# Performance work log

Measured on AMD Instinct MI355X. Metric: run time of the kernel, lower is better.

## Reference

```python
import jax, jax.numpy as jnp
import numpy as np

B, S, SQ, N, DIN, H, A, O = 32, 1024, 32, 128, 128, 256, 100, 2000
MEM_COUNT, ANS_COUNT = 3, 2


def _gru_cell(x, h, w_ih, w_hh, b_ih, b_hh):
    # PyTorch GRUCell math
    gi = x @ w_ih.T + b_ih
    gh = h @ w_hh.T + b_hh
    i_r, i_z, i_n = jnp.split(gi, 3, axis=-1)
    h_r, h_z, h_n = jnp.split(gh, 3, axis=-1)
    r = jax.nn.sigmoid(i_r + h_r)
    z = jax.nn.sigmoid(i_z + h_z)
    n = jnp.tanh(i_n + r * h_n)
    return (1.0 - z) * n + z * h


def _gru_seq(x, h0, w_ih, w_hh, b_ih, b_hh):
    def step(h, xt):
        hn = _gru_cell(xt, h, w_ih, w_hh, b_ih, b_hh)
        return hn, hn
    hT, ys = jax.lax.scan(step, h0, jnp.swapaxes(x, 0, 1))
    return jnp.swapaxes(ys, 0, 1), hT


def setup_inputs() -> dict:
    key = jax.random.key(0)
    ks = iter(jax.random.split(key, 40))
    def U(shape, a=0.05):
        return jax.random.uniform(next(ks), shape, minval=-a, maxval=a, dtype=jnp.float32)
    inp = {}
    inp['c'] = jax.random.normal(next(ks), (B, S, DIN), dtype=jnp.float32)
    inp['q'] = jax.random.normal(next(ks), (B, SQ, DIN), dtype=jnp.float32)
    inp['i_state'] = jnp.zeros((1, B, H), jnp.float32)
    inp['q_state'] = jnp.zeros((1, B, H), jnp.float32)
    for p in ['in', 'qe']:
        inp[p + '_w_ih'] = U((3 * H, DIN)); inp[p + '_w_hh'] = U((3 * H, H))
        inp[p + '_b_ih'] = U((3 * H,)); inp[p + '_b_hh'] = U((3 * H,))
    inp['att_weight'] = U((H, H))
    inp['att_w1'] = U((A, 7 * H + 2)); inp['att_b1'] = U((A,))
    inp['att_w2'] = U((1, A)); inp['att_b2'] = U((1,))
    inp['mem_w_ih'] = U((3 * H, H)); inp['mem_w_hh'] = U((3 * H, H))
    inp['mem_b_ih'] = U((3 * H,)); inp['mem_b_hh'] = U((3 * H,))
    inp['out_w'] = U((O, H)); inp['out_b'] = U((O,))
    inp['ans_w_ih'] = U((3 * H, O + H)); inp['ans_w_hh'] = U((3 * H, H))
    inp['ans_b_ih'] = U((3 * H,)); inp['ans_b_hh'] = U((3 * H,))
    inp['c_index'] = jnp.sort(jax.random.randint(next(ks), (B, N), 0, S), axis=1)
    inp['len_c'] = jax.random.randint(next(ks), (B,), 1, N + 1)
    return inp


def reference(c, q, i_state, q_state, in_w_ih, in_w_hh, in_b_ih, in_b_hh,
              qe_w_ih, qe_w_hh, qe_b_ih, qe_b_hh, att_weight,
              att_w1, att_b1, att_w2, att_b2,
              mem_w_ih, mem_w_hh, mem_b_ih, mem_b_hh,
              out_w, out_b, ans_w_ih, ans_w_hh, ans_b_ih, ans_b_hh,
              c_index, len_c):
    # input / question GRU encoders (dropout omitted: eval mode)
    c_out, _ = _gru_seq(c, i_state[0], in_w_ih, in_w_hh, in_b_ih, in_b_hh)
    _, q_hT = _gru_seq(q, q_state[0], qe_w_ih, qe_w_hh, qe_b_ih, qe_b_hh)
    q_h = q_hT[:, None, :]                                   # [B,1,H]
    # gather sentence-end hidden states: [B,N,H]
    c_sel = jnp.take_along_axis(c_out, c_index[:, :, None], axis=1)
    n_sent = c_index.shape[1]
    mask = jnp.arange(n_sent)[None, :] < len_c[:, None]      # [B,N]
    cw = c_sel @ att_weight                                   # [B,N,H] (fixed across hops)
    m = q_h
    att_list = []
    for _ in range(MEM_COUNT):
        dot_q = (cw * q_h).sum(-1)                            # [B,N]
        dot_m = (cw * m).sum(-1)                              # [B,N]
        feats = jnp.concatenate([
            c_sel, jnp.broadcast_to(m, c_sel.shape), jnp.broadcast_to(q_h, c_sel.shape),
            c_sel * q_h, c_sel * m, jnp.abs(c_sel - q_h), jnp.abs(c_sel - m),
            dot_q[..., None], dot_m[..., None]], axis=2)      # [B,N,7H+2]
        h1 = jnp.tanh(feats @ att_w1.T + att_b1)
        scores = (h1 @ att_w2.T + att_b2)[..., 0]             # [B,N]
        p = jax.nn.softmax(jnp.where(mask, scores, -jnp.inf), axis=1)
        p = jnp.where(mask, p, 0.0)                           # zero-pad like pad_sequence
        att_list.append(p[..., None])
        e = (c_sel * p[..., None]).sum(1)                     # [B,H]
        m = _gru_cell(e, m[:, 0, :], mem_w_ih, mem_w_hh, mem_b_ih, mem_b_hh)[:, None, :]
    msq = m[:, 0, :]
    for _ in range(ANS_COUNT):
        y = jax.nn.softmax(msq @ out_w.T + out_b, axis=1)
        msq = _gru_cell(jnp.concatenate([y, q_hT], axis=1), msq,
                        ans_w_ih, ans_w_hh, ans_b_ih, ans_b_hh)
    y = jax.nn.softmax(msq @ out_w.T + out_b, axis=1)
    return y, jnp.stack(att_list)
```

## Files before the change

### kernel.cpp

```cpp
#include <hip/hip_runtime.h>
#include <cstdint>
#include <cstddef>

typedef short bf16x8 __attribute__((ext_vector_type(8)));
typedef float f32x4 __attribute__((ext_vector_type(4)));
typedef int   i32x4 __attribute__((ext_vector_type(4)));

#define DEV static __device__ __forceinline__

DEV unsigned short f2bf(float x){
  union{float f; unsigned int u;} v; v.f = x;
  unsigned int r = (v.u + 0x7FFFu + ((v.u>>16)&1u)) >> 16;
  return (unsigned short)r;
}
DEV float bf2f(unsigned short h){
  union{unsigned int u; float f;} v; v.u = ((unsigned int)h)<<16;
  return v.f;
}
DEV float bfsel(int dw, int hi){
  union{unsigned int u; float f;} v;
  v.u = hi ? ((unsigned int)dw & 0xFFFF0000u) : ((unsigned int)dw << 16);
  return v.f;
}
DEV float sigm_f(float x){ return __builtin_amdgcn_rcpf(1.0f + __expf(-x)); }
DEV float tanh_f(float x){ return 2.0f*__builtin_amdgcn_rcpf(1.0f + __expf(-2.0f*x)) - 1.0f; }

__global__ void k_f2bf(const float* __restrict__ src, unsigned short* __restrict__ dst, int n){
  int i = blockIdx.x*256 + threadIdx.x;
  if(i<n) dst[i] = f2bf(src[i]);
}

__global__ void k_transpose(const float* __restrict__ in, float* __restrict__ out, int R, int C){
  int i = blockIdx.x*256 + threadIdx.x;
  if(i < R*C){ int r = i/C, c = i - r*C; out[(size_t)c*R + r] = in[i]; }
}

__global__ void k_attw1(const float* __restrict__ w1, unsigned short* __restrict__ dst){
  int i = blockIdx.x*256 + threadIdx.x;
  if(i < 128*1824){
    int r = i/1824, cc = i - r*1824;
    float v = (r<100 && cc<1794)? w1[r*1794 + cc] : 0.0f;
    dst[i] = f2bf(v);
  }
}

__global__ void k_attwT(const float* __restrict__ aw, unsigned short* __restrict__ dst){
  int i = blockIdx.x*256 + threadIdx.x;
  if(i<65536){ int n = i>>8, k = i&255; dst[i] = f2bf(aw[k*256 + n]); }
}

__global__ void k_b1pad(const float* __restrict__ b1, float* __restrict__ dst){
  int i = threadIdx.x; if(i<128) dst[i] = (i<100)? b1[i] : 0.0f;
}

__global__ void k_copy(const float* __restrict__ s, float* __restrict__ d, int n){
  int i = blockIdx.x*256+threadIdx.x; if(i<n) d[i]=s[i];
}

__global__ __launch_bounds__(256) void k_gemm_bf16(
    const unsigned short* __restrict__ A, const unsigned short* __restrict__ Bt,
    int K, const float* __restrict__ bias, int act,
    float* __restrict__ outf, unsigned short* __restrict__ outbf, int ldc)
{
  int lane = threadIdx.x & 63, wave = threadIdx.x >> 6;
  int m_base = blockIdx.x*64 + (wave>>1)*32;
  int n_base = blockIdx.y*64 + (wave&1)*32;
  int cl = lane & 15, q4 = lane >> 4;
  f32x4 acc00={0.f,0.f,0.f,0.f}, acc01=acc00, acc10=acc00, acc11=acc00;
  const int kf_n = K >> 5;
  for(int kf=0; kf<kf_n; kf++){
    int ko = kf*32 + q4*8;
    bf16x8 a0 = *(const bf16x8*)(A + (size_t)(m_base+cl)*K + ko);
    bf16x8 a1 = *(const bf16x8*)(A + (size_t)(m_base+16+cl)*K + ko);
    bf16x8 b0 = *(const bf16x8*)(Bt + (size_t)(n_base+cl)*K + ko);
    bf16x8 b1 = *(const bf16x8*)(Bt + (size_t)(n_base+16+cl)*K + ko);
    acc00 = __builtin_amdgcn_mfma_f32_16x16x32_bf16(a0,b0,acc00,0,0,0);
    acc01 = __builtin_amdgcn_mfma_f32_16x16x32_bf16(a0,b1,acc01,0,0,0);
    acc10 = __builtin_amdgcn_mfma_f32_16x16x32_bf16(a1,b0,acc10,0,0,0);
    acc11 = __builtin_amdgcn_mfma_f32_16x16x32_bf16(a1,b1,acc11,0,0,0);
  }
  #pragma unroll
  for(int mt=0; mt<2; mt++){
    #pragma unroll
    for(int nt=0; nt<2; nt++){
      f32x4 av = (mt==0)? (nt==0?acc00:acc01) : (nt==0?acc10:acc11);
      int col = n_base + nt*16 + cl;
      float bv = bias? bias[col] : 0.0f;
      #pragma unroll
      for(int r=0;r<4;r++){
        int row = m_base + mt*16 + q4*4 + r;
        float v = av[r] + bv;
        if(act) v = tanh_f(v);
        if(outbf) outbf[(size_t)row*ldc + col] = f2bf(v);
        else      outf [(size_t)row*ldc + col] = v;
      }
    }
  }
}

__global__ __launch_bounds__(256) void k_gemm_gi(
    const unsigned short* __restrict__ A, const unsigned short* __restrict__ Bt,
    const float* __restrict__ bias, unsigned short* __restrict__ gi_out, int ss)
{
  int lane = threadIdx.x & 63, wave = threadIdx.x >> 6;
  int m_base = blockIdx.x*64 + (wave>>1)*32;
  int n_base = blockIdx.y*64 + (wave&1)*32;
  int cl = lane & 15, q4 = lane >> 4;
  f32x4 acc00={0.f,0.f,0.f,0.f}, acc01=acc00, acc10=acc00, acc11=acc00;
  for(int kf=0; kf<4; kf++){
    int ko = kf*32 + q4*8;
    bf16x8 a0 = *(const bf16x8*)(A + (size_t)(m_base+cl)*128 + ko);
    bf16x8 a1 = *(const bf16x8*)(A + (size_t)(m_base+16+cl)*128 + ko);
    bf16x8 b0 = *(const bf16x8*)(Bt + (size_t)(n_base+cl)*128 + ko);
    bf16x8 b1 = *(const bf16x8*)(Bt + (size_t)(n_base+16+cl)*128 + ko);
    acc00 = __builtin_amdgcn_mfma_f32_16x16x32_bf16(a0,b0,acc00,0,0,0);
    acc01 = __builtin_amdgcn_mfma_f32_16x16x32_bf16(a0,b1,acc01,0,0,0);
    acc10 = __builtin_amdgcn_mfma_f32_16x16x32_bf16(a1,b0,acc10,0,0,0);
    acc11 = __builtin_amdgcn_mfma_f32_16x16x32_bf16(a1,b1,acc11,0,0,0);
  }
  const int tmask = (1<<ss) - 1;
  #pragma unroll
  for(int mt=0; mt<2; mt++){
    #pragma unroll
    for(int nt=0; nt<2; nt++){
      f32x4 av = (mt==0)? (nt==0?acc00:acc01) : (nt==0?acc10:acc11);
      int col = n_base + nt*16 + cl;
      float bv = bias[col];
      int g = col >> 8, rem = col & 255;
      int w = rem >> 5, s = (rem>>4)&1, cl2 = rem & 15;
      #pragma unroll
      for(int r=0;r<4;r++){
        int arow = m_base + mt*16 + q4*4 + r;
        int t = arow & tmask, b = arow >> ss;
        int blk = b >> 4, brow = b & 15;
        int lane2 = (brow>>2)*16 + cl2, rc = brow & 3;
        size_t idx = ((((size_t)t*2 + blk)*8 + w)*64 + lane2)*24 + g*8 + s*4 + rc;
        gi_out[idx] = f2bf(av[r] + bv);
      }
    }
  }
}

__global__ __launch_bounds__(512,1) void k_gru_rec(
    const unsigned short* __restrict__ whh_c, const unsigned short* __restrict__ whh_q,
    const unsigned short* __restrict__ gi_c,  const unsigned short* __restrict__ gi_q,
    const float* __restrict__ bhh_c, const float* __restrict__ bhh_q,
    const float* __restrict__ h0_c,  const float* __restrict__ h0_q,
    float* __restrict__ c_out, float* __restrict__ q_hT)
{
  __shared__ unsigned short hb0[16*264];
  __shared__ unsigned short hb1[16*264];

  const int blk = blockIdx.x;
  const bool isq = blk >= 2;
  const int cls = isq? blk-2 : blk;
  const int b0 = cls * 16;
  const unsigned short* W  = isq? whh_q : whh_c;
  const unsigned short* GI = isq? gi_q  : gi_c;
  const float* bhh = isq? bhh_q : bhh_c;
  const float* h0  = isq? h0_q  : h0_c;
  const int steps  = isq? 32 : 1024;

  const int tid = threadIdx.x;
  const int lane = tid & 63, wave = tid >> 6;
  const int cl = lane & 15, q4 = lane >> 4;

  bf16x8 Bf[3][2][8];
  #pragma unroll
  for(int g=0; g<3; g++)
    #pragma unroll
    for(int s=0; s<2; s++){
      const unsigned short* wrow = W + (size_t)(g*256 + wave*32 + s*16 + cl)*256;
      #pragma unroll
      for(int kf=0; kf<8; kf++)
        Bf[g][s][kf] = *(const bf16x8*)(wrow + kf*32 + q4*8);
    }

  float bR[2], bZ[2], bN[2];
  #pragma unroll
  for(int s=0; s<2; s++){
    const int col = wave*32 + s*16 + cl;
    bR[s] = bhh[col]; bZ[s] = bhh[256+col]; bN[s] = bhh[512+col];
  }

  float hreg[2][4];
  #pragma unroll
  for(int s=0; s<2; s++){
    const int col = wave*32 + s*16 + cl;
    #pragma unroll
    for(int r=0; r<4; r++){
      const int row = q4*4 + r;
      float v = h0[(size_t)(b0+row)*256 + col];
      hreg[s][r] = v;
      hb0[row*264 + col] = f2bf(v);
    }
  }
  __syncthreads();

  unsigned short* hb_rd = hb0;
  unsigned short* hb_wr = hb1;

  const unsigned short* gi_lane = GI + (((size_t)cls*8 + wave)*64 + lane)*24;
  const size_t gi_tstride = (size_t)2*8*64*24;

  for(int t=0; t<steps; t++){
    const unsigned short* gp = gi_lane + (size_t)t*gi_tstride;
    i32x4 G0 = *(const i32x4*)(gp);
    i32x4 G1 = *(const i32x4*)(gp + 8);
    i32x4 G2 = *(const i32x4*)(gp + 16);

    if(!isq && t>0){
      #pragma unroll
      for(int s=0; s<2; s++){
        const int col = wave*32 + s*16 + cl;
        #pragma unroll
        for(int r=0; r<4; r++)
          c_out[((size_t)(b0+q4*4+r)*1024 + (t-1))*256 + col] = hreg[s][r];
      }
    }

    f32x4 acc[3][2];
    #pragma unroll
    for(int g=0; g<3; g++)
      #pragma unroll
      for(int s=0; s<2; s++){ f32x4 z={0.f,0.f,0.f,0.f}; acc[g][s]=z; }
    #pragma unroll
    for(int kf=0; kf<8; kf++){
      bf16x8 a = *(const bf16x8*)&hb_rd[cl*264 + kf*32 + q4*8];
      #pragma unroll
      for(int g=0; g<3; g++)
        #pragma unroll
        for(int s=0; s<2; s++)
          acc[g][s] = __builtin_amdgcn_mfma_f32_16x16x32_bf16(a, Bf[g][s][kf], acc[g][s], 0,0,0);
    }

    #pragma unroll
    for(int s=0; s<2; s++){
      const int col = wave*32 + s*16 + cl;
      #pragma unroll
      for(int r=0; r<4; r++){
        const int row = q4*4 + r;
        const int k = s*4 + r;
        float gir = bfsel(G0[k>>1], k&1);
        float giz = bfsel(G1[k>>1], k&1);
        float gin = bfsel(G2[k>>1], k&1);
        float rr = sigm_f(gir + acc[0][s][r] + bR[s]);
        float zz = sigm_f(giz + acc[1][s][r] + bZ[s]);
        float nn = tanh_f(gin + rr*(acc[2][s][r] + bN[s]));
        float x  = nn + zz*(hreg[s][r] - nn);
        hreg[s][r] = x;
        hb_wr[row*264 + col] = f2bf(x);
      }
    }
    __syncthreads();
    unsigned short* tmp = hb_rd; hb_rd = hb_wr; hb_wr = tmp;
  }

  #pragma unroll
  for(int s=0; s<2; s++){
    const int col = wave*32 + s*16 + cl;
    #pragma unroll
    for(int r=0; r<4; r++){
      const int row = q4*4 + r;
      if(!isq) c_out[((size_t)(b0+row)*1024 + (steps-1))*256 + col] = hreg[s][r];
      else     q_hT[(size_t)(b0+row)*256 + col] = hreg[s][r];
    }
  }
}

__global__ void k_gather(const float* __restrict__ c_out, const int* __restrict__ c_index,
                         float* __restrict__ c_sel, unsigned short* __restrict__ c_sel_bf){
  int row = blockIdx.x;
  int b = row >> 7, s = row & 127;
  int idx = c_index[b*128 + s];
  float v = c_out[((size_t)b*1024 + idx)*256 + threadIdx.x];
  c_sel   [(size_t)row*256 + threadIdx.x] = v;
  c_sel_bf[(size_t)row*256 + threadIdx.x] = f2bf(v);
}

__global__ void k_feats(const float* __restrict__ c_sel, const float* __restrict__ cw,
                        const float* __restrict__ m_, const float* __restrict__ qh,
                        unsigned short* __restrict__ feats){
  int row = blockIdx.x, tid = threadIdx.x;
  int b = row >> 7;
  float cs  = c_sel[(size_t)row*256 + tid];
  float mj  = m_[b*256 + tid];
  float qj  = qh[b*256 + tid];
  float cwj = cw[(size_t)row*256 + tid];
  float dq = cwj*qj, dm = cwj*mj;
  #pragma unroll
  for(int o=32;o>0;o>>=1){ dq += __shfl_down(dq,o); dm += __shfl_down(dm,o); }
  __shared__ float rq[4], rm[4];
  int lane = tid&63, wave=tid>>6;
  if(lane==0){ rq[wave]=dq; rm[wave]=dm; }
  __syncthreads();
  unsigned short* fr = feats + (size_t)row*1824;
  fr[tid]      = f2bf(cs);
  fr[256+tid]  = f2bf(mj);
  fr[512+tid]  = f2bf(qj);
  fr[768+tid]  = f2bf(cs*qj);
  fr[1024+tid] = f2bf(cs*mj);
  fr[1280+tid] = f2bf(fabsf(cs-qj));
  fr[1536+tid] = f2bf(fabsf(cs-mj));
  if(tid==0){
    float DQ = rq[0]+rq[1]+rq[2]+rq[3];
    float DM = rm[0]+rm[1]+rm[2]+rm[3];
    fr[1792]=f2bf(DQ); fr[1793]=f2bf(DM);
  }
  if(tid<30) fr[1794+tid]=0;
}

__global__ void k_scores(const float* __restrict__ h1, const float* __restrict__ w2,
                         const float* __restrict__ b2, float* __restrict__ scores){
  int row = blockIdx.x*4 + (threadIdx.x>>6);
  int lane = threadIdx.x & 63;
  float v = 0.0f;
  if(lane < 100)    v += h1[(size_t)row*128 + lane]*w2[lane];
  if(lane+64 < 100) v += h1[(size_t)row*128 + lane+64]*w2[lane+64];
  #pragma unroll
  for(int o=32;o>0;o>>=1) v += __shfl_down(v,o);
  if(lane==0) scores[row] = v + b2[0];
}

__global__ void k_softmax_e(const float* __restrict__ scores, const int* __restrict__ len_c,
                            const float* __restrict__ c_sel, float* __restrict__ out_att,
                            float* __restrict__ e){
  __shared__ float red[256];
  __shared__ float p[128];
  int b = blockIdx.x, tid = threadIdx.x;
  int L = len_c[b];
  float s = -1e30f;
  if(tid<128 && tid<L) s = scores[b*128+tid];
  red[tid]=s; __syncthreads();
  for(int o=128;o>0;o>>=1){ if(tid<o) red[tid]=fmaxf(red[tid],red[tid+o]); __syncthreads(); }
  float mx = red[0]; __syncthreads();
  float ex = (tid<128 && tid<L)? __expf(s-mx) : 0.0f;
  red[tid]=ex; __syncthreads();
  for(int o=128;o>0;o>>=1){ if(tid<o) red[tid]+=red[tid+o]; __syncthreads(); }
  float inv = 1.0f/red[0];
  if(tid<128){ float pv = ex*inv; p[tid]=pv; out_att[b*128+tid]=pv; }
  __syncthreads();
  float acc = 0.0f;
  for(int si=0; si<128; si++) acc += p[si]*c_sel[((size_t)b*128+si)*256 + tid];
  e[b*256+tid] = acc;
}

__global__ void k_gru_cell(const float* __restrict__ x1, int len1,
                           const float* __restrict__ x2, int len2,
                           const float* __restrict__ hprev,
                           const float* __restrict__ wihT, const float* __restrict__ whhT,
                           const float* __restrict__ bih, const float* __restrict__ bhh,
                           float* __restrict__ hout){
  __shared__ float xs[2304];
  __shared__ float hs[256];
  int m = blockIdx.x, tid = threadIdx.x;
  int Kx = len1 + len2;
  for(int i=tid;i<len1;i+=256) xs[i] = x1[(size_t)m*len1 + i];
  for(int i=tid;i<len2;i+=256) xs[len1+i] = x2[(size_t)m*len2 + i];
  hs[tid] = hprev[m*256 + tid];
  __syncthreads();
  float ar=0, az=0, an=0;
  for(int k=0;k<Kx;k++){
    float xv = xs[k];
    const float* wr = wihT + (size_t)k*768;
    ar += xv*wr[tid]; az += xv*wr[256+tid]; an += xv*wr[512+tid];
  }
  float gr=0, gz=0, gn=0;
  for(int k=0;k<256;k++){
    float hv = hs[k];
    const float* wr = whhT + (size_t)k*768;
    gr += hv*wr[tid]; gz += hv*wr[256+tid]; gn += hv*wr[512+tid];
  }
  float rr = sigm_f(ar + bih[tid]     + gr + bhh[tid]);
  float zz = sigm_f(az + bih[256+tid] + gz + bhh[256+tid]);
  float nn = tanh_f(an + bih[512+tid] + rr*(gn + bhh[512+tid]));
  hout[m*256+tid] = (1.0f-zz)*nn + zz*hs[tid];
}

__global__ void k_logits(const float* __restrict__ msq, const float* __restrict__ out_wT,
                         const float* __restrict__ out_b, float* __restrict__ ylin){
  int i = blockIdx.x*256 + threadIdx.x;
  if(i >= 32*2000) return;
  int mrow = i/2000, n = i - mrow*2000;
  float acc = out_b[n];
  const float* mr = msq + mrow*256;
  for(int k=0;k<256;k++) acc += mr[k]*out_wT[(size_t)k*2000 + n];
  ylin[i] = acc;
}

__global__ void k_softmax_o(const float* __restrict__ x, float* __restrict__ y){
  __shared__ float red[256];
  int b = blockIdx.x, tid = threadIdx.x;
  const float* xr = x + (size_t)b*2000;
  float mx = -1e30f;
  for(int i=tid;i<2000;i+=256) mx = fmaxf(mx, xr[i]);
  red[tid]=mx; __syncthreads();
  for(int o=128;o>0;o>>=1){ if(tid<o) red[tid]=fmaxf(red[tid],red[tid+o]); __syncthreads(); }
  mx = red[0]; __syncthreads();
  float sum=0.0f;
  for(int i=tid;i<2000;i+=256) sum += __expf(xr[i]-mx);
  red[tid]=sum; __syncthreads();
  for(int o=128;o>0;o>>=1){ if(tid<o) red[tid]+=red[tid+o]; __syncthreads(); }
  float inv = 1.0f/red[0];
  for(int i=tid;i<2000;i+=256) y[(size_t)b*2000+i] = __expf(xr[i]-mx)*inv;
}

extern "C" void kernel_launch(void* const* d_in, const int* in_sizes, int n_in,
                              void* d_out, int out_size, void* d_ws, size_t ws_size,
                              hipStream_t stream)
{
  const float* c        = (const float*)d_in[0];
  const float* q        = (const float*)d_in[1];
  const float* i_state  = (const float*)d_in[2];
  const float* q_state  = (const float*)d_in[3];
  const float* in_w_ih  = (const float*)d_in[4];
  const float* in_w_hh  = (const float*)d_in[5];
  const float* in_b_ih  = (const float*)d_in[6];
  const float* in_b_hh  = (const float*)d_in[7];
  const float* qe_w_ih  = (const float*)d_in[8];
  const float* qe_w_hh  = (const float*)d_in[9];
  const float* qe_b_ih  = (const float*)d_in[10];
  const float* qe_b_hh  = (const float*)d_in[11];
  const float* att_weight = (const float*)d_in[12];
  const float* att_w1   = (const float*)d_in[13];
  const float* att_b1   = (const float*)d_in[14];
  const float* att_w2   = (const float*)d_in[15];
  const float* att_b2   = (const float*)d_in[16];
  const float* mem_w_ih = (const float*)d_in[17];
  const float* mem_w_hh = (const float*)d_in[18];
  const float* mem_b_ih = (const float*)d_in[19];
  const float* mem_b_hh = (const float*)d_in[20];
  const float* out_w    = (const float*)d_in[21];
  const float* out_b    = (const float*)d_in[22];
  const float* ans_w_ih = (const float*)d_in[23];
  const float* ans_w_hh = (const float*)d_in[24];
  const float* ans_b_ih = (const float*)d_in[25];
  const float* ans_b_hh = (const float*)d_in[26];
  const int*   c_index  = (const int*)d_in[27];
  const int*   len_c    = (const int*)d_in[28];
  float* outp = (float*)d_out;

  char* wp = (char*)d_ws;
  auto take = [&](size_t nbytes)->char*{
    char* p = wp; wp += (nbytes + 255) & ~(size_t)255; return p;
  };
  unsigned short* c_bf      = (unsigned short*)take((size_t)32*1024*128*2);
  unsigned short* q_bf      = (unsigned short*)take((size_t)32*32*128*2);
  unsigned short* wih_in_bf = (unsigned short*)take(768*128*2);
  unsigned short* wih_qe_bf = (unsigned short*)take(768*128*2);
  unsigned short* whh_in_bf = (unsigned short*)take(768*256*2);
  unsigned short* whh_qe_bf = (unsigned short*)take(768*256*2);
  unsigned short* attwT_bf  = (unsigned short*)take(256*256*2);
  unsigned short* attw1_bf  = (unsigned short*)take(128*1824*2);
  float* b1pad              = (float*)take(128*4);
  float* out_wT             = (float*)take((size_t)256*2000*4);
  float* mem_wihT           = (float*)take(256*768*4);
  float* mem_whhT           = (float*)take(256*768*4);
  float* ans_wihT           = (float*)take((size_t)2256*768*4);
  float* ans_whhT           = (float*)take(256*768*4);
  unsigned short* gi_c_bf   = (unsigned short*)take((size_t)32768*768*2);
  unsigned short* gi_q_bf   = (unsigned short*)take((size_t)1024*768*2);
  float* c_out              = (float*)take((size_t)32*1024*256*4);
  float* q_hT               = (float*)take(32*256*4);
  float* c_sel              = (float*)take((size_t)4096*256*4);
  unsigned short* c_sel_bf  = (unsigned short*)take((size_t)4096*256*2);
  float* cw                 = (float*)take((size_t)4096*256*4);
  unsigned short* feats_bf  = (unsigned short*)take((size_t)4096*1824*2);
  float* h1                 = (float*)take((size_t)4096*128*4);
  float* scores             = (float*)take(4096*4);
  float* e_buf              = (float*)take(32*256*4);
  float* m_buf              = (float*)take(32*256*4);
  float* msq                = (float*)take(32*256*4);
  float* ylin               = (float*)take((size_t)32*2000*4);
  float* ybuf               = (float*)take((size_t)32*2000*4);

  k_f2bf<<<16384,256,0,stream>>>(c, c_bf, 32*1024*128);
  k_f2bf<<<512,256,0,stream>>>(q, q_bf, 32*32*128);
  k_f2bf<<<384,256,0,stream>>>(in_w_ih, wih_in_bf, 768*128);
  k_f2bf<<<384,256,0,stream>>>(qe_w_ih, wih_qe_bf, 768*128);
  k_f2bf<<<768,256,0,stream>>>(in_w_hh, whh_in_bf, 768*256);
  k_f2bf<<<768,256,0,stream>>>(qe_w_hh, whh_qe_bf, 768*256);
  k_attwT<<<256,256,0,stream>>>(att_weight, attwT_bf);
  k_attw1<<<912,256,0,stream>>>(att_w1, attw1_bf);
  k_b1pad<<<1,128,0,stream>>>(att_b1, b1pad);
  k_transpose<<<2000,256,0,stream>>>(out_w, out_wT, 2000, 256);
  k_transpose<<<768,256,0,stream>>>(mem_w_ih, mem_wihT, 768, 256);
  k_transpose<<<768,256,0,stream>>>(mem_w_hh, mem_whhT, 768, 256);
  k_transpose<<<6768,256,0,stream>>>(ans_w_ih, ans_wihT, 768, 2256);
  k_transpose<<<768,256,0,stream>>>(ans_w_hh, ans_whhT, 768, 256);

  k_gemm_gi<<<dim3(512,12),256,0,stream>>>(c_bf, wih_in_bf, in_b_ih, gi_c_bf, 10);
  k_gemm_gi<<<dim3(16,12),256,0,stream>>>(q_bf, wih_qe_bf, qe_b_ih, gi_q_bf, 5);

  k_gru_rec<<<4,512,0,stream>>>(whh_in_bf, whh_qe_bf, gi_c_bf, gi_q_bf,
                                in_b_hh, qe_b_hh, i_state, q_state, c_out, q_hT);

  k_gather<<<4096,256,0,stream>>>(c_out, c_index, c_sel, c_sel_bf);
  k_gemm_bf16<<<dim3(64,4),256,0,stream>>>(c_sel_bf, attwT_bf, 256, nullptr, 0, cw, nullptr, 256);
  k_copy<<<32,256,0,stream>>>(q_hT, m_buf, 32*256);

  for(int it=0; it<3; it++){
    k_feats<<<4096,256,0,stream>>>(c_sel, cw, m_buf, q_hT, feats_bf);
    k_gemm_bf16<<<dim3(64,2),256,0,stream>>>(feats_bf, attw1_bf, 1824, b1pad, 1, h1, nullptr, 128);
    k_scores<<<1024,256,0,stream>>>(h1, att_w2, att_b2, scores);
    k_softmax_e<<<32,256,0,stream>>>(scores, len_c, c_sel, outp + 64000 + it*4096, e_buf);
    k_gru_cell<<<32,256,0,stream>>>(e_buf, 256, nullptr, 0, m_buf,
                                    mem_wihT, mem_whhT, mem_b_ih, mem_b_hh, m_buf);
  }

  k_copy<<<32,256,0,stream>>>(m_buf, msq, 32*256);
  for(int it=0; it<2; it++){
    k_logits<<<250,256,0,stream>>>(msq, out_wT, out_b, ylin);
    k_softmax_o<<<32,256,0,stream>>>(ylin, ybuf);
    k_gru_cell<<<32,256,0,stream>>>(ybuf, 2000, q_hT, 256, msq,
                                    ans_wihT, ans_whhT, ans_b_ih, ans_b_hh, msq);
  }
  k_logits<<<250,256,0,stream>>>(msq, out_wT, out_b, ylin);
  k_softmax_o<<<32,256,0,stream>>>(ylin, outp);
}
```

Baseline: 3.052 ms.

## Fold hidden r/z biases into input GEMM, store r/z gates in fp32

The input-projection GEMM now adds the hidden-side r and z biases and writes the r/z gate pre-activations as fp32 in a separate buffer, with the n gate kept as bf16. This removes per-step bias adds and bf16 unpacking for r/z inside the serial recurrence. The recurrence also converts its bf16 hidden-state stores two values at a time, and the workspace now aliases the gate buffers with the later attention buffers. In exchange, each recurrence step reads more gate data from memory and the input GEMM writes more bytes.

```diff
diff --git a/kernel.cpp b/kernel.cpp
--- a/kernel.cpp
+++ b/kernel.cpp
@@ -1,4 +1,5 @@
 #include <hip/hip_runtime.h>
+#include <hip/hip_bf16.h>
 #include <cstdint>
 #include <cstddef>
 
@@ -100,7 +101,8 @@
 
 __global__ __launch_bounds__(256) void k_gemm_gi(
     const unsigned short* __restrict__ A, const unsigned short* __restrict__ Bt,
-    const float* __restrict__ bias, unsigned short* __restrict__ gi_out, int ss)
+    const float* __restrict__ bih, const float* __restrict__ bhh,
+    float* __restrict__ rz_out, unsigned short* __restrict__ n_out, int ss)
 {
   int lane = threadIdx.x & 63, wave = threadIdx.x >> 6;
   int m_base = blockIdx.x*64 + (wave>>1)*32;
@@ -125,17 +127,19 @@
     for(int nt=0; nt<2; nt++){
       f32x4 av = (mt==0)? (nt==0?acc00:acc01) : (nt==0?acc10:acc11);
       int col = n_base + nt*16 + cl;
-      float bv = bias[col];
+      float bi = bih[col];
       int g = col >> 8, rem = col & 255;
       int w = rem >> 5, s = (rem>>4)&1, cl2 = rem & 15;
+      float bh = (g<2)? bhh[col] : 0.0f;
       #pragma unroll
       for(int r=0;r<4;r++){
         int arow = m_base + mt*16 + q4*4 + r;
         int t = arow & tmask, b = arow >> ss;
         int blk = b >> 4, brow = b & 15;
         int lane2 = (brow>>2)*16 + cl2, rc = brow & 3;
-        size_t idx = ((((size_t)t*2 + blk)*8 + w)*64 + lane2)*24 + g*8 + s*4 + rc;
-        gi_out[idx] = f2bf(av[r] + bv);
+        size_t L = ((((size_t)t*2 + blk)*8 + w)*64 + lane2);
+        if(g < 2) rz_out[L*16 + g*8 + s*4 + rc] = av[r] + bi + bh;
+        else      n_out [L*8  + s*4 + rc]       = f2bf(av[r] + bi);
       }
     }
   }
@@ -143,7 +147,8 @@
 
 __global__ __launch_bounds__(512,1) void k_gru_rec(
     const unsigned short* __restrict__ whh_c, const unsigned short* __restrict__ whh_q,
-    const unsigned short* __restrict__ gi_c,  const unsigned short* __restrict__ gi_q,
+    const float* __restrict__ rz_c, const unsigned short* __restrict__ n_c,
+    const float* __restrict__ rz_q, const unsigned short* __restrict__ n_q,
     const float* __restrict__ bhh_c, const float* __restrict__ bhh_q,
     const float* __restrict__ h0_c,  const float* __restrict__ h0_q,
     float* __restrict__ c_out, float* __restrict__ q_hT)
@@ -156,7 +161,8 @@
   const int cls = isq? blk-2 : blk;
   const int b0 = cls * 16;
   const unsigned short* W  = isq? whh_q : whh_c;
-  const unsigned short* GI = isq? gi_q  : gi_c;
+  const float* RZ = isq? rz_q : rz_c;
+  const unsigned short* NG = isq? n_q : n_c;
   const float* bhh = isq? bhh_q : bhh_c;
   const float* h0  = isq? h0_q  : h0_c;
   const int steps  = isq? 32 : 1024;
@@ -176,11 +182,11 @@
         Bf[g][s][kf] = *(const bf16x8*)(wrow + kf*32 + q4*8);
     }
 
-  float bR[2], bZ[2], bN[2];
+  float bN[2];
   #pragma unroll
   for(int s=0; s<2; s++){
     const int col = wave*32 + s*16 + cl;
-    bR[s] = bhh[col]; bZ[s] = bhh[256+col]; bN[s] = bhh[512+col];
+    bN[s] = bhh[512+col];
   }
 
   float hreg[2][4];
@@ -200,14 +206,18 @@
   unsigned short* hb_rd = hb0;
   unsigned short* hb_wr = hb1;
 
-  const unsigned short* gi_lane = GI + (((size_t)cls*8 + wave)*64 + lane)*24;
-  const size_t gi_tstride = (size_t)2*8*64*24;
+  const float* rz_lane = RZ + (((size_t)cls*8 + wave)*64 + lane)*16;
+  const unsigned short* n_lane = NG + (((size_t)cls*8 + wave)*64 + lane)*8;
+  const size_t rz_tstride = (size_t)2*8*64*16;
+  const size_t n_tstride  = (size_t)2*8*64*8;
 
   for(int t=0; t<steps; t++){
-    const unsigned short* gp = gi_lane + (size_t)t*gi_tstride;
-    i32x4 G0 = *(const i32x4*)(gp);
-    i32x4 G1 = *(const i32x4*)(gp + 8);
-    i32x4 G2 = *(const i32x4*)(gp + 16);
+    const float* rzp = rz_lane + (size_t)t*rz_tstride;
+    f32x4 Gr0 = *(const f32x4*)(rzp);
+    f32x4 Gr1 = *(const f32x4*)(rzp + 4);
+    f32x4 Gz0 = *(const f32x4*)(rzp + 8);
+    f32x4 Gz1 = *(const f32x4*)(rzp + 12);
+    i32x4 Nw  = *(const i32x4*)(n_lane + (size_t)t*n_tstride);
 
     if(!isq && t>0){
       #pragma unroll
@@ -237,19 +247,25 @@
     #pragma unroll
     for(int s=0; s<2; s++){
       const int col = wave*32 + s*16 + cl;
+      float x4[4];
       #pragma unroll
       for(int r=0; r<4; r++){
-        const int row = q4*4 + r;
         const int k = s*4 + r;
-        float gir = bfsel(G0[k>>1], k&1);
-        float giz = bfsel(G1[k>>1], k&1);
-        float gin = bfsel(G2[k>>1], k&1);
-        float rr = sigm_f(gir + acc[0][s][r] + bR[s]);
-        float zz = sigm_f(giz + acc[1][s][r] + bZ[s]);
+        float rr = sigm_f((s? Gr1[r] : Gr0[r]) + acc[0][s][r]);
+        float zz = sigm_f((s? Gz1[r] : Gz0[r]) + acc[1][s][r]);
+        float gin = bfsel(Nw[k>>1], k&1);
         float nn = tanh_f(gin + rr*(acc[2][s][r] + bN[s]));
         float x  = nn + zz*(hreg[s][r] - nn);
         hreg[s][r] = x;
-        hb_wr[row*264 + col] = f2bf(x);
+        x4[r] = x;
+      }
+      #pragma unroll
+      for(int p=0; p<2; p++){
+        __hip_bfloat162 bb = __float22bfloat162_rn(make_float2(x4[2*p], x4[2*p+1]));
+        union{ __hip_bfloat162 b; unsigned int u; } cvt; cvt.b = bb;
+        const int row = q4*4 + 2*p;
+        hb_wr[row*264 + col]     = (unsigned short)(cvt.u & 0xFFFFu);
+        hb_wr[(row+1)*264 + col] = (unsigned short)(cvt.u >> 16);
       }
     }
     __syncthreads();
@@ -458,16 +474,21 @@
   float* mem_whhT           = (float*)take(256*768*4);
   float* ans_wihT           = (float*)take((size_t)2256*768*4);
   float* ans_whhT           = (float*)take(256*768*4);
-  unsigned short* gi_c_bf   = (unsigned short*)take((size_t)32768*768*2);
-  unsigned short* gi_q_bf   = (unsigned short*)take((size_t)1024*768*2);
+
+  char* region = take((size_t)86507520);
+  float*          gi_rz_c = (float*)(region);
+  unsigned short* gi_n_c  = (unsigned short*)(region + 67108864);
+  float*          gi_rz_q = (float*)(region + 83886080);
+  unsigned short* gi_n_q  = (unsigned short*)(region + 85983232);
+  float*          c_sel    = (float*)(region);
+  unsigned short* c_sel_bf = (unsigned short*)(region + 4194304);
+  float*          cw       = (float*)(region + 6291456);
+  unsigned short* feats_bf = (unsigned short*)(region + 10485760);
+  float*          h1       = (float*)(region + 25427968);
+  float*          scores   = (float*)(region + 27525120);
+
   float* c_out              = (float*)take((size_t)32*1024*256*4);
   float* q_hT               = (float*)take(32*256*4);
-  float* c_sel              = (float*)take((size_t)4096*256*4);
-  unsigned short* c_sel_bf  = (unsigned short*)take((size_t)4096*256*2);
-  float* cw                 = (float*)take((size_t)4096*256*4);
-  unsigned short* feats_bf  = (unsigned short*)take((size_t)4096*1824*2);
-  float* h1                 = (float*)take((size_t)4096*128*4);
-  float* scores             = (float*)take(4096*4);
   float* e_buf              = (float*)take(32*256*4);
   float* m_buf              = (float*)take(32*256*4);
   float* msq                = (float*)take(32*256*4);
@@ -489,10 +510,10 @@
   k_transpose<<<6768,256,0,stream>>>(ans_w_ih, ans_wihT, 768, 2256);
   k_transpose<<<768,256,0,stream>>>(ans_w_hh, ans_whhT, 768, 256);
 
-  k_gemm_gi<<<dim3(512,12),256,0,stream>>>(c_bf, wih_in_bf, in_b_ih, gi_c_bf, 10);
-  k_gemm_gi<<<dim3(16,12),256,0,stream>>>(q_bf, wih_qe_bf, qe_b_ih, gi_q_bf, 5);
-
-  k_gru_rec<<<4,512,0,stream>>>(whh_in_bf, whh_qe_bf, gi_c_bf, gi_q_bf,
+  k_gemm_gi<<<dim3(512,12),256,0,stream>>>(c_bf, wih_in_bf, in_b_ih, in_b_hh, gi_rz_c, gi_n_c, 10);
+  k_gemm_gi<<<dim3(16,12),256,0,stream>>>(q_bf, wih_qe_bf, qe_b_ih, qe_b_hh, gi_rz_q, gi_n_q, 5);
+
+  k_gru_rec<<<4,512,0,stream>>>(whh_in_bf, whh_qe_bf, gi_rz_c, gi_n_c, gi_rz_q, gi_n_q,
                                 in_b_hh, qe_b_hh, i_state, q_state, c_out, q_hT);
 
   k_gather<<<4096,256,0,stream>>>(c_out, c_index, c_sel, c_sel_bf);
```

Result: slower. 3.831 ms (+25.5%).
